# Kernel tuning notes

Measured on AMD Instinct MI355X. Metric: run time of the kernel, lower is better.

The kernel has to match this reference:

```python
import jax, jax.numpy as jnp
import numpy as np

H = 16  # n_heads

def setup_inputs() -> dict:
    key = jax.random.key(0)
    ks = jax.random.split(key, 11)
    B, L, D = 2, 2048, 1024
    w = 1.0 / np.sqrt(D).astype(np.float32)
    return {
        "query": jax.random.normal(ks[0], (B, L, D), jnp.float32),
        "key":   jax.random.normal(ks[1], (B, L, D), jnp.float32),
        "value": jax.random.normal(ks[2], (B, L, D), jnp.float32),
        "Wq": jax.random.normal(ks[3], (D, D), jnp.float32) * w,
        "bq": jax.random.normal(ks[4], (D,), jnp.float32) * 0.01,
        "Wk": jax.random.normal(ks[5], (D, D), jnp.float32) * w,
        "bk": jax.random.normal(ks[6], (D,), jnp.float32) * 0.01,
        "Wv": jax.random.normal(ks[7], (D, D), jnp.float32) * w,
        "bv": jax.random.normal(ks[8], (D,), jnp.float32) * 0.01,
        "Wo": jax.random.normal(ks[9], (D, D), jnp.float32) * w,
        "bo": jax.random.normal(ks[10], (D,), jnp.float32) * 0.01,
        "masksize": 256,
    }

def reference(query, key, value, Wq, bq, Wk, bk, Wv, bv, Wo, bo, masksize):
    B, L, D = query.shape
    d_k = D // H
    scale = 1.0 / np.sqrt(d_k).astype(np.float32)

    def proj(x, W, b):
        # nn.Linear: x @ W.T + b, then [B,L,H,d_k] -> [B,H,L,d_k]
        return (x @ W.T + b).reshape(B, L, H, d_k).transpose(0, 2, 1, 3)

    q = proj(query, Wq, bq)
    k = proj(key, Wk, bk)
    v = proj(value, Wv, bv)

    # Sliding-window float mask (faithful to original: a 0/1 FLOAT tensor is
    # passed as attn_mask to SDPA, so it is ADDED to scores, not -inf-masked).
    half = masksize // 2
    i = jnp.arange(L)[:, None]
    j = jnp.arange(L)[None, :]
    band = (jnp.abs(i - j) <= half).astype(q.dtype)  # [L, L]

    scores = jnp.einsum('bhqd,bhkd->bhqk', q, k) * scale + band  # [B,H,L,L]
    attn = jax.nn.softmax(scores, axis=-1)
    out = jnp.einsum('bhqk,bhkd->bhqd', attn, v)  # [B,H,L,d_k]
    out = out.transpose(0, 2, 1, 3).reshape(B, L, D)
    return out @ Wo.T + bo
```

## Files before the change

kernel.cpp:

```cpp
#include <hip/hip_runtime.h>
#include <hip/hip_bf16.h>

#define Hh 16
#define Ll 2048
#define Dd 1024
#define DK 64
#define Mm 4096
#define Kk 1024
#define Nn 1024

typedef short bf16x8 __attribute__((ext_vector_type(8)));
typedef float f32x4 __attribute__((ext_vector_type(4)));

static __device__ __forceinline__ unsigned short f2bf(float f) {
    union { __hip_bfloat16 b; unsigned short u; } cv;
    cv.b = __float2bfloat16(f);
    return cv.u;
}

static __device__ __forceinline__ unsigned pack_bf2(float a, float b) {
    union { __hip_bfloat162 h; unsigned u; } cv;
    cv.h = __float22bfloat162_rn(make_float2(a, b));
    return cv.u;
}

static __device__ __forceinline__ float fexp2(float x) {
    return __builtin_amdgcn_exp2f(x);
}

static __device__ __forceinline__ void glds16(const ushort* g, ushort* l) {
    __builtin_amdgcn_global_load_lds((const __attribute__((address_space(1))) unsigned int*)g,
                                     (__attribute__((address_space(3))) unsigned int*)l,
                                     16, 0, 0);
}

__global__ __launch_bounds__(256) void cast_all(
    const float* __restrict__ q, const float* __restrict__ k, const float* __restrict__ v,
    const float* __restrict__ wq, const float* __restrict__ wk, const float* __restrict__ wv,
    const float* __restrict__ wo,
    ushort* __restrict__ qb, ushort* __restrict__ kb, ushort* __restrict__ vb,
    ushort* __restrict__ wqb, ushort* __restrict__ wkb, ushort* __restrict__ wvb,
    ushort* __restrict__ wob) {
    const int bx = blockIdx.x;
    const float4* s; ushort4* d; int base;
    if      (bx <  4096) { s = (const float4*)q;  d = (ushort4*)qb;  base = 0; }
    else if (bx <  8192) { s = (const float4*)k;  d = (ushort4*)kb;  base = 4096; }
    else if (bx < 12288) { s = (const float4*)v;  d = (ushort4*)vb;  base = 8192; }
    else if (bx < 13312) { s = (const float4*)wq; d = (ushort4*)wqb; base = 12288; }
    else if (bx < 14336) { s = (const float4*)wk; d = (ushort4*)wkb; base = 13312; }
    else if (bx < 15360) { s = (const float4*)wv; d = (ushort4*)wvb; base = 14336; }
    else                 { s = (const float4*)wo; d = (ushort4*)wob; base = 15360; }
    const int i = (bx - base) * 256 + threadIdx.x;
    float4 vv = s[i];
    ushort4 o;
    o.x = f2bf(vv.x); o.y = f2bf(vv.y); o.z = f2bf(vv.z); o.w = f2bf(vv.w);
    d[i] = o;
}

__global__ __launch_bounds__(256) void gemm_qkv(
    const ushort* __restrict__ A0, const ushort* __restrict__ A1, const ushort* __restrict__ A2,
    const ushort* __restrict__ W0, const ushort* __restrict__ W1, const ushort* __restrict__ W2,
    const float* __restrict__ b0, const float* __restrict__ b1, const float* __restrict__ b2,
    ushort* __restrict__ O0, ushort* __restrict__ O1, ushort* __restrict__ OVt) {
    __shared__ __align__(16) ushort SM[2 * 128 * 32];
    ushort* As = SM;
    ushort* Bs = SM + 4096;
    const int z = blockIdx.z;
    const ushort* A = (z == 0) ? A0 : (z == 1) ? A1 : A2;
    const ushort* W = (z == 0) ? W0 : (z == 1) ? W1 : W2;
    const float* bias = (z == 0) ? b0 : (z == 1) ? b1 : b2;

    const int t = threadIdx.x;
    const int wave = t >> 6, lane = t & 63;
    const int quad = lane >> 4, l15 = lane & 15;
    const int brow = blockIdx.y * 128, bcol = blockIdx.x * 128;
    const int wr = (wave >> 1) * 64, wc = (wave & 1) * 64;
    const int gr = wave * 16 + (lane >> 2);
    const int gc = (lane & 3) * 8;

    f32x4 acc[4][4] = {};

    for (int k0 = 0; k0 < Kk; k0 += 32) {
        __syncthreads();
        glds16(A + (size_t)(brow + gr) * Kk + k0 + gc,      As + wave * 512);
        glds16(A + (size_t)(brow + 64 + gr) * Kk + k0 + gc, As + 2048 + wave * 512);
        glds16(W + (size_t)(bcol + gr) * Kk + k0 + gc,      Bs + wave * 512);
        glds16(W + (size_t)(bcol + 64 + gr) * Kk + k0 + gc, Bs + 2048 + wave * 512);
        __syncthreads();

        bf16x8 af[4], bfr[4];
#pragma unroll
        for (int i = 0; i < 4; i++)
            af[i] = *(const bf16x8*)(As + (wr + i * 16 + l15) * 32 + quad * 8);
#pragma unroll
        for (int j = 0; j < 4; j++)
            bfr[j] = *(const bf16x8*)(Bs + (wc + j * 16 + l15) * 32 + quad * 8);
#pragma unroll
        for (int i = 0; i < 4; i++)
#pragma unroll
            for (int j = 0; j < 4; j++)
                acc[i][j] = __builtin_amdgcn_mfma_f32_16x16x32_bf16(af[i], bfr[j], acc[i][j], 0, 0, 0);
    }

    if (z < 2) {
        ushort* Out = (z == 0) ? O0 : O1;
        const float oscl = (z == 0) ? 0.18033688f : 1.0f;
#pragma unroll
        for (int i = 0; i < 4; i++)
#pragma unroll
            for (int j = 0; j < 4; j++) {
                const int n = bcol + wc + j * 16 + l15;
                const float bv = bias[n];
                const int h = n >> 6, dk = n & 63;
#pragma unroll
                for (int r = 0; r < 4; r++) {
                    const int m = brow + wr + i * 16 + quad * 4 + r;
                    const int b = m >> 11, l = m & 2047;
                    Out[((size_t)(b * Hh + h) * Ll + l) * DK + dk] = f2bf((acc[i][j][r] + bv) * oscl);
                }
            }
    } else {
        ushort* T = SM;
        const int b = brow >> 11;
        const int lbase = brow & 2047;
        const int npr = (wave & 1) * 16 + l15;
#pragma unroll
        for (int j = 0; j < 4; j++) {
            __syncthreads();
            const float bv = bias[bcol + wc + j * 16 + l15];
#pragma unroll
            for (int i = 0; i < 4; i++)
#pragma unroll
                for (int r = 0; r < 4; r++) {
                    const int m = wr + i * 16 + quad * 4 + r;
                    T[npr * 136 + m] = f2bf(acc[i][j][r] + bv);
                }
            __syncthreads();
#pragma unroll
            for (int cc = 0; cc < 2; cc++) {
                const int idx = t + cc * 256;
                const int ni = idx >> 4;
                const int ms = idx & 15;
                const int n = bcol + (ni >> 4) * 64 + j * 16 + (ni & 15);
                const int hh = n >> 6, dk = n & 63;
                uint4 val = *(const uint4*)(T + ni * 136 + ms * 8);
                *(uint4*)(OVt + ((size_t)(b * Hh + hh) * DK + dk) * Ll + lbase + ms * 8) = val;
            }
        }
    }
}

__global__ __launch_bounds__(256) void attn_kernel(const ushort* __restrict__ Q,
                                                   const ushort* __restrict__ Kp,
                                                   const ushort* __restrict__ Vt,
                                                   ushort* __restrict__ Oout,
                                                   const int* __restrict__ masksize) {
    __shared__ __align__(16) ushort Ks[2 * 128 * 32];
    __shared__ __align__(16) ushort Vs[64 * 128];
    const int t = threadIdx.x;
    const int wave = t >> 6, lane = t & 63;
    const int quad = lane >> 4, l15 = lane & 15;
    const int bx = blockIdx.x;
    const int bh = bx & 31, qc = bx >> 5;
    const int q0w = qc * 128 + wave * 32;
    const int half = masksize[0] >> 1;
    const unsigned wid = (unsigned)(2 * half);

    const ushort* Qb = Q + (size_t)bh * (Ll * DK);
    const ushort* Kb = Kp + (size_t)bh * (Ll * DK);
    const ushort* Vb = Vt + (size_t)bh * (DK * Ll);

    const bf16x8 qA0 = *(const bf16x8*)(Qb + (size_t)(q0w + l15) * DK + quad * 8);
    const bf16x8 qA1 = *(const bf16x8*)(Qb + (size_t)(q0w + l15) * DK + 32 + quad * 8);
    const bf16x8 qB0 = *(const bf16x8*)(Qb + (size_t)(q0w + 16 + l15) * DK + quad * 8);
    const bf16x8 qB1 = *(const bf16x8*)(Qb + (size_t)(q0w + 16 + l15) * DK + 32 + quad * 8);

    const float C2IN  = (1.0f - 24.0f) * 1.44269504088896f;
    const float C2OUT = -24.0f * 1.44269504088896f;

    f32x4 OA[4] = {}, OB[4] = {};
    float rsA = 0.f, rsB = 0.f;

    const int krow = lane >> 2;
    const int kcol8 = (lane & 3) * 8;
    const int vdl = lane >> 4;
    const int vg0 = 2 * (lane & 15);

    for (int kt = 0; kt < Ll; kt += 128) {
        __syncthreads();
        if (wave < 2) {
            const int cbase = wave * 4;
#pragma unroll
            for (int c = 0; c < 4; c++)
#pragma unroll
                for (int pan = 0; pan < 2; pan++)
                    glds16(Kb + (size_t)(kt + (cbase + c) * 16 + krow) * DK + pan * 32 + kcol8,
                           Ks + (pan * 128 + (cbase + c) * 16) * 32);
        } else {
            const int sb = (wave - 2) * 8;
#pragma unroll
            for (int i = 0; i < 8; i++) {
                const int sidx = sb + i;
                const int d = sidx * 4 + vdl;
                const int g0 = vg0 ^ (d & 30);
                glds16(Vb + (size_t)d * Ll + kt + g0 * 4, Vs + sidx * 512);
            }
        }
        __syncthreads();

        const int qlo = q0w, qhi = q0w + 31;
        const bool allout = (kt + 127 < qlo - half) || (kt > qhi + half);
        const bool allin  = (kt >= qhi - half) && (kt + 127 <= qlo + half);

#pragma unroll
        for (int s = 0; s < 4; s++) {
            const bf16x8 kf00 = *(const bf16x8*)(Ks + ((2 * s) * 16 + l15) * 32 + quad * 8);
            const bf16x8 kf01 = *(const bf16x8*)(Ks + 4096 + ((2 * s) * 16 + l15) * 32 + quad * 8);
            const bf16x8 kf10 = *(const bf16x8*)(Ks + ((2 * s + 1) * 16 + l15) * 32 + quad * 8);
            const bf16x8 kf11 = *(const bf16x8*)(Ks + 4096 + ((2 * s + 1) * 16 + l15) * 32 + quad * 8);
            f32x4 zA0 = {}, zA1 = {}, zB0 = {}, zB1 = {};
            zA0 = __builtin_amdgcn_mfma_f32_16x16x32_bf16(kf00, qA0, zA0, 0, 0, 0);
            zA0 = __builtin_amdgcn_mfma_f32_16x16x32_bf16(kf01, qA1, zA0, 0, 0, 0);
            zA1 = __builtin_amdgcn_mfma_f32_16x16x32_bf16(kf10, qA0, zA1, 0, 0, 0);
            zA1 = __builtin_amdgcn_mfma_f32_16x16x32_bf16(kf11, qA1, zA1, 0, 0, 0);
            zB0 = __builtin_amdgcn_mfma_f32_16x16x32_bf16(kf00, qB0, zB0, 0, 0, 0);
            zB0 = __builtin_amdgcn_mfma_f32_16x16x32_bf16(kf01, qB1, zB0, 0, 0, 0);
            zB1 = __builtin_amdgcn_mfma_f32_16x16x32_bf16(kf10, qB0, zB1, 0, 0, 0);
            zB1 = __builtin_amdgcn_mfma_f32_16x16x32_bf16(kf11, qB1, zB1, 0, 0, 0);

            float pA[8], pB[8];
            if (allin || allout) {
                const float cu = allin ? C2IN : C2OUT;
#pragma unroll
                for (int g = 0; g < 2; g++)
#pragma unroll
                    for (int r = 0; r < 4; r++) {
                        pA[g * 4 + r] = fexp2((g ? zA1[r] : zA0[r]) + cu);
                        pB[g * 4 + r] = fexp2((g ? zB1[r] : zB0[r]) + cu);
                    }
            } else {
                const int kb = kt + s * 32 + quad * 4 + half;
#pragma unroll
                for (int g = 0; g < 2; g++)
#pragma unroll
                    for (int r = 0; r < 4; r++) {
                        const unsigned ttA = (unsigned)(kb + g * 16 + r - (q0w + l15));
                        const unsigned ttB = (unsigned)(kb + g * 16 + r - (q0w + 16 + l15));
                        pA[g * 4 + r] = fexp2((g ? zA1[r] : zA0[r]) + (ttA <= wid ? C2IN : C2OUT));
                        pB[g * 4 + r] = fexp2((g ? zB1[r] : zB0[r]) + (ttB <= wid ? C2IN : C2OUT));
                    }
            }
#pragma unroll
            for (int j = 0; j < 8; j++) { rsA += pA[j]; rsB += pB[j]; }

            bf16x8 pfA, pfB;
            ((unsigned*)&pfA)[0] = pack_bf2(pA[0], pA[1]);
            ((unsigned*)&pfA)[1] = pack_bf2(pA[2], pA[3]);
            ((unsigned*)&pfA)[2] = pack_bf2(pA[4], pA[5]);
            ((unsigned*)&pfA)[3] = pack_bf2(pA[6], pA[7]);
            ((unsigned*)&pfB)[0] = pack_bf2(pB[0], pB[1]);
            ((unsigned*)&pfB)[1] = pack_bf2(pB[2], pB[3]);
            ((unsigned*)&pfB)[2] = pack_bf2(pB[4], pB[5]);
            ((unsigned*)&pfB)[3] = pack_bf2(pB[6], pB[7]);

#pragma unroll
            for (int i = 0; i < 4; i++) {
                const int d = i * 16 + l15;
                const int x4 = (d & 30) * 4;
                const int bi = d * 128;
                const ushort4 v1 = *(const ushort4*)(Vs + bi + (((s * 8 + quad) * 4) ^ x4));
                const ushort4 v2 = *(const ushort4*)(Vs + bi + (((s * 8 + 4 + quad) * 4) ^ x4));
                bf16x8 vc;
                *(ushort4*)&vc = v1;
                *((ushort4*)&vc + 1) = v2;
                OA[i] = __builtin_amdgcn_mfma_f32_16x16x32_bf16(pfA, vc, OA[i], 0, 0, 0);
                OB[i] = __builtin_amdgcn_mfma_f32_16x16x32_bf16(pfB, vc, OB[i], 0, 0, 0);
            }
        }
    }

    rsA += __shfl_xor(rsA, 16); rsA += __shfl_xor(rsA, 32);
    rsB += __shfl_xor(rsB, 16); rsB += __shfl_xor(rsB, 32);
    float liA[4], liB[4];
#pragma unroll
    for (int r = 0; r < 4; r++) {
        liA[r] = 1.0f / __shfl(rsA, quad * 4 + r);
        liB[r] = 1.0f / __shfl(rsB, quad * 4 + r);
    }

    const int b = bh >> 4, h = bh & 15;
#pragma unroll
    for (int i = 0; i < 4; i++)
#pragma unroll
        for (int r = 0; r < 4; r++) {
            const int qa = q0w + quad * 4 + r;
            Oout[((size_t)b * Ll + qa) * Dd + h * DK + i * 16 + l15] = f2bf(OA[i][r] * liA[r]);
            Oout[((size_t)b * Ll + qa + 16) * Dd + h * DK + i * 16 + l15] = f2bf(OB[i][r] * liB[r]);
        }
}

__global__ __launch_bounds__(256) void gemm_o(const ushort* __restrict__ A,
                                              const ushort* __restrict__ W,
                                              const float* __restrict__ bias,
                                              float* __restrict__ Out) {
    __shared__ __align__(16) ushort As[64 * 32];
    __shared__ __align__(16) ushort Bs[128 * 32];
    const int t = threadIdx.x;
    const int wave = t >> 6, lane = t & 63;
    const int quad = lane >> 4, l15 = lane & 15;
    const int brow = blockIdx.y * 64, bcol = blockIdx.x * 128;
    const int wr = (wave >> 1) * 32, wc = (wave & 1) * 64;
    const int gr = wave * 16 + (lane >> 2);
    const int gc = (lane & 3) * 8;

    f32x4 acc[2][4] = {};

    for (int k0 = 0; k0 < Kk; k0 += 32) {
        __syncthreads();
        glds16(A + (size_t)(brow + gr) * Kk + k0 + gc,      As + wave * 512);
        glds16(W + (size_t)(bcol + gr) * Kk + k0 + gc,      Bs + wave * 512);
        glds16(W + (size_t)(bcol + 64 + gr) * Kk + k0 + gc, Bs + 2048 + wave * 512);
        __syncthreads();

        bf16x8 af[2], bfr[4];
#pragma unroll
        for (int i = 0; i < 2; i++)
            af[i] = *(const bf16x8*)(As + (wr + i * 16 + l15) * 32 + quad * 8);
#pragma unroll
        for (int j = 0; j < 4; j++)
            bfr[j] = *(const bf16x8*)(Bs + (wc + j * 16 + l15) * 32 + quad * 8);
#pragma unroll
        for (int i = 0; i < 2; i++)
#pragma unroll
            for (int j = 0; j < 4; j++)
                acc[i][j] = __builtin_amdgcn_mfma_f32_16x16x32_bf16(af[i], bfr[j], acc[i][j], 0, 0, 0);
    }

#pragma unroll
    for (int i = 0; i < 2; i++)
#pragma unroll
        for (int j = 0; j < 4; j++) {
            const int n = bcol + wc + j * 16 + l15;
            const float bv = bias[n];
#pragma unroll
            for (int r = 0; r < 4; r++) {
                const int m = brow + wr + i * 16 + quad * 4 + r;
                Out[(size_t)m * Nn + n] = acc[i][j][r] + bv;
            }
        }
}

extern "C" void kernel_launch(void* const* d_in, const int* in_sizes, int n_in,
                              void* d_out, int out_size, void* d_ws, size_t ws_size,
                              hipStream_t stream) {
    const float* query = (const float*)d_in[0];
    const float* key   = (const float*)d_in[1];
    const float* value = (const float*)d_in[2];
    const float* Wq = (const float*)d_in[3];
    const float* bq = (const float*)d_in[4];
    const float* Wk = (const float*)d_in[5];
    const float* bk = (const float*)d_in[6];
    const float* Wv = (const float*)d_in[7];
    const float* bv = (const float*)d_in[8];
    const float* Wo = (const float*)d_in[9];
    const float* bo = (const float*)d_in[10];
    const int* masksize = (const int*)d_in[11];

    char* ws = (char*)d_ws;
    const size_t MB = 1024 * 1024;
    ushort* qb  = (ushort*)(ws + 0 * MB);
    ushort* kbf = (ushort*)(ws + 8 * MB);
    ushort* vbf = (ushort*)(ws + 16 * MB);
    ushort* wqb = (ushort*)(ws + 24 * MB);
    ushort* wkb = (ushort*)(ws + 26 * MB);
    ushort* wvb = (ushort*)(ws + 28 * MB);
    ushort* wob = (ushort*)(ws + 30 * MB);
    ushort* Qp  = (ushort*)(ws + 32 * MB);
    ushort* Kp  = (ushort*)(ws + 40 * MB);
    ushort* Vt  = (ushort*)(ws + 48 * MB);
    ushort* AO  = (ushort*)(ws + 56 * MB);

    cast_all<<<16384, 256, 0, stream>>>(query, key, value, Wq, Wk, Wv, Wo,
                                        qb, kbf, vbf, wqb, wkb, wvb, wob);

    gemm_qkv<<<dim3(8, 32, 3), 256, 0, stream>>>(qb, kbf, vbf,
                                                 wqb, wkb, wvb,
                                                 bq, bk, bv,
                                                 Qp, Kp, Vt);

    attn_kernel<<<512, 256, 0, stream>>>(Qp, Kp, Vt, AO, masksize);

    gemm_o<<<dim3(8, 64), 256, 0, stream>>>(AO, wob, bo, (float*)d_out);
}
```

Baseline: 230.9 us.

## Halve attention block size and fold mask constant into MFMA accumulator init

The attention kernel now runs 1024 blocks of 128 threads, each covering 64 query rows instead of 128. The K/V tile loading is reassigned so one wave loads K and the other loads V. The softmax shift constant is preloaded into the MFMA accumulator instead of being added before each exp2. In partially masked tiles, in-band scores are multiplied by e rather than picking a per-element additive constant. Row sums use a pairwise tree. The smaller blocks are meant to improve scheduling granularity, at the cost of each K/V tile being loaded from global memory by twice as many blocks.

```diff
diff --git a/kernel.cpp b/kernel.cpp
--- a/kernel.cpp
+++ b/kernel.cpp
@@ -150,7 +150,7 @@
     }
 }
 
-__global__ __launch_bounds__(256) void attn_kernel(const ushort* __restrict__ Q,
+__global__ __launch_bounds__(128) void attn_kernel(const ushort* __restrict__ Q,
                                                    const ushort* __restrict__ Kp,
                                                    const ushort* __restrict__ Vt,
                                                    ushort* __restrict__ Oout,
@@ -162,7 +162,7 @@
     const int quad = lane >> 4, l15 = lane & 15;
     const int bx = blockIdx.x;
     const int bh = bx & 31, qc = bx >> 5;
-    const int q0w = qc * 128 + wave * 32;
+    const int q0w = qc * 64 + wave * 32;
     const int half = masksize[0] >> 1;
     const unsigned wid = (unsigned)(2 * half);
 
@@ -177,6 +177,7 @@
 
     const float C2IN  = (1.0f - 24.0f) * 1.44269504088896f;
     const float C2OUT = -24.0f * 1.44269504088896f;
+    const float E1 = 2.718281828f;
 
     f32x4 OA[4] = {}, OB[4] = {};
     float rsA = 0.f, rsB = 0.f;
@@ -188,22 +189,19 @@
 
     for (int kt = 0; kt < Ll; kt += 128) {
         __syncthreads();
-        if (wave < 2) {
-            const int cbase = wave * 4;
-#pragma unroll
-            for (int c = 0; c < 4; c++)
+        if (wave == 0) {
+#pragma unroll
+            for (int c = 0; c < 8; c++)
 #pragma unroll
                 for (int pan = 0; pan < 2; pan++)
-                    glds16(Kb + (size_t)(kt + (cbase + c) * 16 + krow) * DK + pan * 32 + kcol8,
-                           Ks + (pan * 128 + (cbase + c) * 16) * 32);
+                    glds16(Kb + (size_t)(kt + c * 16 + krow) * DK + pan * 32 + kcol8,
+                           Ks + (pan * 128 + c * 16) * 32);
         } else {
-            const int sb = (wave - 2) * 8;
-#pragma unroll
-            for (int i = 0; i < 8; i++) {
-                const int sidx = sb + i;
-                const int d = sidx * 4 + vdl;
+#pragma unroll
+            for (int i = 0; i < 16; i++) {
+                const int d = i * 4 + vdl;
                 const int g0 = vg0 ^ (d & 30);
-                glds16(Vb + (size_t)d * Ll + kt + g0 * 4, Vs + sidx * 512);
+                glds16(Vb + (size_t)d * Ll + kt + g0 * 4, Vs + i * 512);
             }
         }
         __syncthreads();
@@ -211,6 +209,9 @@
         const int qlo = q0w, qhi = q0w + 31;
         const bool allout = (kt + 127 < qlo - half) || (kt > qhi + half);
         const bool allin  = (kt >= qhi - half) && (kt + 127 <= qlo + half);
+        const bool uniform = allin || allout;
+        const float cinit = allin ? C2IN : C2OUT;
+        f32x4 cvec = {cinit, cinit, cinit, cinit};
 
 #pragma unroll
         for (int s = 0; s < 4; s++) {
@@ -218,25 +219,23 @@
             const bf16x8 kf01 = *(const bf16x8*)(Ks + 4096 + ((2 * s) * 16 + l15) * 32 + quad * 8);
             const bf16x8 kf10 = *(const bf16x8*)(Ks + ((2 * s + 1) * 16 + l15) * 32 + quad * 8);
             const bf16x8 kf11 = *(const bf16x8*)(Ks + 4096 + ((2 * s + 1) * 16 + l15) * 32 + quad * 8);
-            f32x4 zA0 = {}, zA1 = {}, zB0 = {}, zB1 = {};
-            zA0 = __builtin_amdgcn_mfma_f32_16x16x32_bf16(kf00, qA0, zA0, 0, 0, 0);
+            f32x4 zA0 = __builtin_amdgcn_mfma_f32_16x16x32_bf16(kf00, qA0, cvec, 0, 0, 0);
             zA0 = __builtin_amdgcn_mfma_f32_16x16x32_bf16(kf01, qA1, zA0, 0, 0, 0);
-            zA1 = __builtin_amdgcn_mfma_f32_16x16x32_bf16(kf10, qA0, zA1, 0, 0, 0);
+            f32x4 zA1 = __builtin_amdgcn_mfma_f32_16x16x32_bf16(kf10, qA0, cvec, 0, 0, 0);
             zA1 = __builtin_amdgcn_mfma_f32_16x16x32_bf16(kf11, qA1, zA1, 0, 0, 0);
-            zB0 = __builtin_amdgcn_mfma_f32_16x16x32_bf16(kf00, qB0, zB0, 0, 0, 0);
+            f32x4 zB0 = __builtin_amdgcn_mfma_f32_16x16x32_bf16(kf00, qB0, cvec, 0, 0, 0);
             zB0 = __builtin_amdgcn_mfma_f32_16x16x32_bf16(kf01, qB1, zB0, 0, 0, 0);
-            zB1 = __builtin_amdgcn_mfma_f32_16x16x32_bf16(kf10, qB0, zB1, 0, 0, 0);
+            f32x4 zB1 = __builtin_amdgcn_mfma_f32_16x16x32_bf16(kf10, qB0, cvec, 0, 0, 0);
             zB1 = __builtin_amdgcn_mfma_f32_16x16x32_bf16(kf11, qB1, zB1, 0, 0, 0);
 
             float pA[8], pB[8];
-            if (allin || allout) {
-                const float cu = allin ? C2IN : C2OUT;
+            if (uniform) {
 #pragma unroll
                 for (int g = 0; g < 2; g++)
 #pragma unroll
                     for (int r = 0; r < 4; r++) {
-                        pA[g * 4 + r] = fexp2((g ? zA1[r] : zA0[r]) + cu);
-                        pB[g * 4 + r] = fexp2((g ? zB1[r] : zB0[r]) + cu);
+                        pA[g * 4 + r] = fexp2(g ? zA1[r] : zA0[r]);
+                        pB[g * 4 + r] = fexp2(g ? zB1[r] : zB0[r]);
                     }
             } else {
                 const int kb = kt + s * 32 + quad * 4 + half;
@@ -246,12 +245,12 @@
                     for (int r = 0; r < 4; r++) {
                         const unsigned ttA = (unsigned)(kb + g * 16 + r - (q0w + l15));
                         const unsigned ttB = (unsigned)(kb + g * 16 + r - (q0w + 16 + l15));
-                        pA[g * 4 + r] = fexp2((g ? zA1[r] : zA0[r]) + (ttA <= wid ? C2IN : C2OUT));
-                        pB[g * 4 + r] = fexp2((g ? zB1[r] : zB0[r]) + (ttB <= wid ? C2IN : C2OUT));
+                        pA[g * 4 + r] = fexp2(g ? zA1[r] : zA0[r]) * (ttA <= wid ? E1 : 1.0f);
+                        pB[g * 4 + r] = fexp2(g ? zB1[r] : zB0[r]) * (ttB <= wid ? E1 : 1.0f);
                     }
             }
-#pragma unroll
-            for (int j = 0; j < 8; j++) { rsA += pA[j]; rsB += pB[j]; }
+            rsA += ((pA[0] + pA[1]) + (pA[2] + pA[3])) + ((pA[4] + pA[5]) + (pA[6] + pA[7]));
+            rsB += ((pB[0] + pB[1]) + (pB[2] + pB[3])) + ((pB[4] + pB[5]) + (pB[6] + pB[7]));
 
             bf16x8 pfA, pfB;
             ((unsigned*)&pfA)[0] = pack_bf2(pA[0], pA[1]);
@@ -388,7 +387,7 @@
                                                  bq, bk, bv,
                                                  Qp, Kp, Vt);
 
-    attn_kernel<<<512, 256, 0, stream>>>(Qp, Kp, Vt, AO, masksize);
+    attn_kernel<<<1024, 128, 0, stream>>>(Qp, Kp, Vt, AO, masksize);
 
     gemm_o<<<dim3(8, 64), 256, 0, stream>>>(AO, wob, bo, (float*)d_out);
 }
```

Measured after the change: 234.2 us. No clear change (+1.4%).

## Fold mask bias into MFMA init, sum softmax rows via ones-MFMA, truncate bf16

Applied to the files above, without the earlier changes.

The QK^T MFMAs now start from an accumulator pre-filled with the bias constant, so the uniform tiles skip a per-element add. Mixed tiles multiply by e instead of selecting a per-element exponent offset. Row sums are computed with an extra MFMA against a ones vector instead of scalar adds and cross-lane shuffles. Probabilities are packed to bf16 by truncation with a byte permute instead of round-to-nearest, which lowers precision slightly and makes the row sums use the truncated values.

```diff
diff --git a/kernel.cpp b/kernel.cpp
--- a/kernel.cpp
+++ b/kernel.cpp
@@ -18,10 +18,9 @@
     return cv.u;
 }
 
-static __device__ __forceinline__ unsigned pack_bf2(float a, float b) {
-    union { __hip_bfloat162 h; unsigned u; } cv;
-    cv.h = __float22bfloat162_rn(make_float2(a, b));
-    return cv.u;
+static __device__ __forceinline__ unsigned packtr(float a, float b) {
+    return __builtin_amdgcn_perm(__builtin_bit_cast(unsigned, b),
+                                 __builtin_bit_cast(unsigned, a), 0x07060302u);
 }
 
 static __device__ __forceinline__ float fexp2(float x) {
@@ -177,9 +176,14 @@
 
     const float C2IN  = (1.0f - 24.0f) * 1.44269504088896f;
     const float C2OUT = -24.0f * 1.44269504088896f;
+    const float E1 = 2.718281828f;
+
+    bf16x8 onesf;
+#pragma unroll
+    for (int j = 0; j < 8; j++) onesf[j] = (short)0x3F80;
 
     f32x4 OA[4] = {}, OB[4] = {};
-    float rsA = 0.f, rsB = 0.f;
+    f32x4 SA = {}, SB = {};
 
     const int krow = lane >> 2;
     const int kcol8 = (lane & 3) * 8;
@@ -211,6 +215,9 @@
         const int qlo = q0w, qhi = q0w + 31;
         const bool allout = (kt + 127 < qlo - half) || (kt > qhi + half);
         const bool allin  = (kt >= qhi - half) && (kt + 127 <= qlo + half);
+        const bool uniform = allin || allout;
+        const float cinit = allin ? C2IN : C2OUT;
+        f32x4 cvec = {cinit, cinit, cinit, cinit};
 
 #pragma unroll
         for (int s = 0; s < 4; s++) {
@@ -218,25 +225,23 @@
             const bf16x8 kf01 = *(const bf16x8*)(Ks + 4096 + ((2 * s) * 16 + l15) * 32 + quad * 8);
             const bf16x8 kf10 = *(const bf16x8*)(Ks + ((2 * s + 1) * 16 + l15) * 32 + quad * 8);
             const bf16x8 kf11 = *(const bf16x8*)(Ks + 4096 + ((2 * s + 1) * 16 + l15) * 32 + quad * 8);
-            f32x4 zA0 = {}, zA1 = {}, zB0 = {}, zB1 = {};
-            zA0 = __builtin_amdgcn_mfma_f32_16x16x32_bf16(kf00, qA0, zA0, 0, 0, 0);
+            f32x4 zA0 = __builtin_amdgcn_mfma_f32_16x16x32_bf16(kf00, qA0, cvec, 0, 0, 0);
             zA0 = __builtin_amdgcn_mfma_f32_16x16x32_bf16(kf01, qA1, zA0, 0, 0, 0);
-            zA1 = __builtin_amdgcn_mfma_f32_16x16x32_bf16(kf10, qA0, zA1, 0, 0, 0);
+            f32x4 zA1 = __builtin_amdgcn_mfma_f32_16x16x32_bf16(kf10, qA0, cvec, 0, 0, 0);
             zA1 = __builtin_amdgcn_mfma_f32_16x16x32_bf16(kf11, qA1, zA1, 0, 0, 0);
-            zB0 = __builtin_amdgcn_mfma_f32_16x16x32_bf16(kf00, qB0, zB0, 0, 0, 0);
+            f32x4 zB0 = __builtin_amdgcn_mfma_f32_16x16x32_bf16(kf00, qB0, cvec, 0, 0, 0);
             zB0 = __builtin_amdgcn_mfma_f32_16x16x32_bf16(kf01, qB1, zB0, 0, 0, 0);
-            zB1 = __builtin_amdgcn_mfma_f32_16x16x32_bf16(kf10, qB0, zB1, 0, 0, 0);
+            f32x4 zB1 = __builtin_amdgcn_mfma_f32_16x16x32_bf16(kf10, qB0, cvec, 0, 0, 0);
             zB1 = __builtin_amdgcn_mfma_f32_16x16x32_bf16(kf11, qB1, zB1, 0, 0, 0);
 
             float pA[8], pB[8];
-            if (allin || allout) {
-                const float cu = allin ? C2IN : C2OUT;
+            if (uniform) {
 #pragma unroll
                 for (int g = 0; g < 2; g++)
 #pragma unroll
                     for (int r = 0; r < 4; r++) {
-                        pA[g * 4 + r] = fexp2((g ? zA1[r] : zA0[r]) + cu);
-                        pB[g * 4 + r] = fexp2((g ? zB1[r] : zB0[r]) + cu);
+                        pA[g * 4 + r] = fexp2(g ? zA1[r] : zA0[r]);
+                        pB[g * 4 + r] = fexp2(g ? zB1[r] : zB0[r]);
                     }
             } else {
                 const int kb = kt + s * 32 + quad * 4 + half;
@@ -246,22 +251,23 @@
                     for (int r = 0; r < 4; r++) {
                         const unsigned ttA = (unsigned)(kb + g * 16 + r - (q0w + l15));
                         const unsigned ttB = (unsigned)(kb + g * 16 + r - (q0w + 16 + l15));
-                        pA[g * 4 + r] = fexp2((g ? zA1[r] : zA0[r]) + (ttA <= wid ? C2IN : C2OUT));
-                        pB[g * 4 + r] = fexp2((g ? zB1[r] : zB0[r]) + (ttB <= wid ? C2IN : C2OUT));
+                        pA[g * 4 + r] = fexp2(g ? zA1[r] : zA0[r]) * (ttA <= wid ? E1 : 1.0f);
+                        pB[g * 4 + r] = fexp2(g ? zB1[r] : zB0[r]) * (ttB <= wid ? E1 : 1.0f);
                     }
             }
-#pragma unroll
-            for (int j = 0; j < 8; j++) { rsA += pA[j]; rsB += pB[j]; }
 
             bf16x8 pfA, pfB;
-            ((unsigned*)&pfA)[0] = pack_bf2(pA[0], pA[1]);
-            ((unsigned*)&pfA)[1] = pack_bf2(pA[2], pA[3]);
-            ((unsigned*)&pfA)[2] = pack_bf2(pA[4], pA[5]);
-            ((unsigned*)&pfA)[3] = pack_bf2(pA[6], pA[7]);
-            ((unsigned*)&pfB)[0] = pack_bf2(pB[0], pB[1]);
-            ((unsigned*)&pfB)[1] = pack_bf2(pB[2], pB[3]);
-            ((unsigned*)&pfB)[2] = pack_bf2(pB[4], pB[5]);
-            ((unsigned*)&pfB)[3] = pack_bf2(pB[6], pB[7]);
+            ((unsigned*)&pfA)[0] = packtr(pA[0], pA[1]);
+            ((unsigned*)&pfA)[1] = packtr(pA[2], pA[3]);
+            ((unsigned*)&pfA)[2] = packtr(pA[4], pA[5]);
+            ((unsigned*)&pfA)[3] = packtr(pA[6], pA[7]);
+            ((unsigned*)&pfB)[0] = packtr(pB[0], pB[1]);
+            ((unsigned*)&pfB)[1] = packtr(pB[2], pB[3]);
+            ((unsigned*)&pfB)[2] = packtr(pB[4], pB[5]);
+            ((unsigned*)&pfB)[3] = packtr(pB[6], pB[7]);
+
+            SA = __builtin_amdgcn_mfma_f32_16x16x32_bf16(pfA, onesf, SA, 0, 0, 0);
+            SB = __builtin_amdgcn_mfma_f32_16x16x32_bf16(pfB, onesf, SB, 0, 0, 0);
 
 #pragma unroll
             for (int i = 0; i < 4; i++) {
@@ -279,13 +285,11 @@
         }
     }
 
-    rsA += __shfl_xor(rsA, 16); rsA += __shfl_xor(rsA, 32);
-    rsB += __shfl_xor(rsB, 16); rsB += __shfl_xor(rsB, 32);
     float liA[4], liB[4];
 #pragma unroll
     for (int r = 0; r < 4; r++) {
-        liA[r] = 1.0f / __shfl(rsA, quad * 4 + r);
-        liB[r] = 1.0f / __shfl(rsB, quad * 4 + r);
+        liA[r] = 1.0f / SA[r];
+        liB[r] = 1.0f / SB[r];
     }
 
     const int b = bh >> 4, h = bh & 15;
```

After: 224.5 us. 2.8% less time.
